# Optimization experiments

Hardware: AMD Instinct MI355X
Metric: run time of the kernel (lower is better)

The kernel has to match this reference:

```python
import jax, jax.numpy as jnp
import numpy as np

B, H, W, C = 8, 28, 28, 1024
NH = 16
HD = C // NH          # head dim 64
HID = 4 * C           # mlp hidden 4096
BC = C // 2           # bottleneck channels 512
SCALE = HD ** -0.5


def setup_inputs() -> dict:
    key = jax.random.key(0)
    ks = iter(jax.random.split(key, 32))
    def rn(shape, s=0.02):
        return jax.random.normal(next(ks), shape, jnp.float32) * s
    return dict(
        x=jax.random.normal(next(ks), (B, H, W, C), jnp.float32),
        norm1_w=jnp.ones((C,), jnp.float32), norm1_b=jnp.zeros((C,), jnp.float32),
        qkv_w=rn((C, 3 * C)), qkv_b=jnp.zeros((3 * C,), jnp.float32),
        proj_w=rn((C, C)), proj_b=jnp.zeros((C,), jnp.float32),
        rel_h=rn((2 * H - 1, HD)), rel_w=rn((2 * W - 1, HD)),
        norm2_w=jnp.ones((C,), jnp.float32), norm2_b=jnp.zeros((C,), jnp.float32),
        fc1_w=rn((C, HID)), fc1_b=jnp.zeros((HID,), jnp.float32),
        fc2_w=rn((HID, C)), fc2_b=jnp.zeros((C,), jnp.float32),
        conv1_w=rn((1, 1, C, BC)), ln1_w=jnp.ones((BC,), jnp.float32), ln1_b=jnp.zeros((BC,), jnp.float32),
        conv2_w=rn((3, 3, BC, BC)), ln2_w=jnp.ones((BC,), jnp.float32), ln2_b=jnp.zeros((BC,), jnp.float32),
        conv3_w=rn((1, 1, BC, C)), ln3_w=rn((C,)), ln3_b=rn((C,)),
    )


def _ln(x, w, b, eps):
    # layernorm over last axis (channels in NHWC)
    m = jnp.mean(x, -1, keepdims=True)
    v = jnp.mean((x - m) ** 2, -1, keepdims=True)
    return (x - m) * jax.lax.rsqrt(v + eps) * w + b


def _conv(x, w, pad):
    return jax.lax.conv_general_dilated(
        x, w, (1, 1), pad, dimension_numbers=('NHWC', 'HWIO', 'NHWC'))


def _gelu(x):
    return jax.nn.gelu(x, approximate=False)


def _block_forward(x, norm1_w, norm1_b, qkv_w, qkv_b, proj_w, proj_b,
                   rel_h, rel_w, norm2_w, norm2_b, fc1_w, fc1_b, fc2_w, fc2_b,
                   conv1_w, ln1_w, ln1_b, conv2_w, ln2_w, ln2_b, conv3_w, ln3_w, ln3_b):
    S = H * W
    shortcut = x
    xn = _ln(x, norm1_w, norm1_b, 1e-5)

    # ---- attention with decomposed relative position bias ----
    qkv = xn.reshape(B, S, C) @ qkv_w + qkv_b                 # [B,S,3C]
    qkv = qkv.reshape(B, S, 3, NH, HD).transpose(2, 0, 3, 1, 4)  # [3,B,nh,S,hd]
    q, k, v = qkv[0], qkv[1], qkv[2]
    attn = jnp.einsum('bnsd,bntd->bnst', q * SCALE, k)        # [B,nh,S,S]

    idx_h = jnp.arange(H)[:, None] - jnp.arange(H)[None, :] + (H - 1)
    idx_w = jnp.arange(W)[:, None] - jnp.arange(W)[None, :] + (W - 1)
    Rh = rel_h[idx_h]   # [H,H,hd]
    Rw = rel_w[idx_w]   # [W,W,hd]
    qr = q.reshape(B, NH, H, W, HD)
    bias_h = jnp.einsum('bnhwd,hkd->bnhwk', qr, Rh)           # [B,nh,H,W,H]
    bias_w = jnp.einsum('bnhwd,wkd->bnhwk', qr, Rw)           # [B,nh,H,W,W]
    attn = (attn.reshape(B, NH, H, W, H, W)
            + bias_h[..., :, None] + bias_w[..., None, :]).reshape(B, NH, S, S)

    attn = jax.nn.softmax(attn, axis=-1)
    out = jnp.einsum('bnst,bntd->bnsd', attn, v)              # [B,nh,S,hd]
    out = out.transpose(0, 2, 1, 3).reshape(B, H, W, C)
    out = out @ proj_w + proj_b

    x = shortcut + out

    # ---- MLP ----
    xn = _ln(x, norm2_w, norm2_b, 1e-5)
    x = x + (_gelu(xn.reshape(B, S, C) @ fc1_w + fc1_b) @ fc2_w + fc2_b).reshape(B, H, W, C)

    # ---- residual bottleneck conv (channel LayerNorm, eps=1e-6) ----
    out = _conv(x, conv1_w, 'VALID')
    out = _gelu(_ln(out, ln1_w, ln1_b, 1e-6))
    out = _conv(out, conv2_w, ((1, 1), (1, 1)))
    out = _gelu(_ln(out, ln2_w, ln2_b, 1e-6))
    out = _conv(out, conv3_w, 'VALID')
    out = _ln(out, ln3_w, ln3_b, 1e-6)
    return x + out


def reference(x, norm1_w, norm1_b, qkv_w, qkv_b, proj_w, proj_b,
              rel_h, rel_w, norm2_w, norm2_b, fc1_w, fc1_b, fc2_w, fc2_b,
              conv1_w, ln1_w, ln1_b, conv2_w, ln2_w, ln2_b, conv3_w, ln3_w, ln3_b):
    return _block_forward(x, norm1_w, norm1_b, qkv_w, qkv_b, proj_w, proj_b,
                          rel_h, rel_w, norm2_w, norm2_b, fc1_w, fc1_b, fc2_w, fc2_b,
                          conv1_w, ln1_w, ln1_b, conv2_w, ln2_w, ln2_b, conv3_w, ln3_w, ln3_b)
```

## Files before the change

kernel.cpp:

```cpp
#include <hip/hip_runtime.h>
#include <cstdint>
#include <cstddef>

using u16 = unsigned short;
using u32 = unsigned int;

__device__ __forceinline__ float bf2f(u16 u){
  union { u32 i; float f; } x; x.i = ((u32)u) << 16; return x.f;
}
__device__ __forceinline__ u16 f2bf(float f){
  union { float f; u32 i; } x; x.f = f;
  u32 r = x.i + 0x7fffu + ((x.i >> 16) & 1u);
  return (u16)(r >> 16);
}
__device__ __forceinline__ float gelu_f(float x){
  return 0.5f * x * (1.0f + erff(x * 0.70710678118654752f));
}
__device__ __forceinline__ void gld16(const void* g, void* l){
  __builtin_amdgcn_global_load_lds((__attribute__((address_space(1))) void*)(void*)g,
                                   (__attribute__((address_space(3))) void*)l, 16, 0, 0);
}

typedef __bf16 bf16x8 __attribute__((ext_vector_type(8)));
typedef float  f32x4  __attribute__((ext_vector_type(4)));

__global__ __launch_bounds__(256) void k_transpose(const float* __restrict__ src,
                                                   u16* __restrict__ dst, int R, int C){
  __shared__ u16 tile[32][33];
  int bx = blockIdx.x * 32;
  int by = blockIdx.y * 32;
  int tx = threadIdx.x & 31;
  int ty = threadIdx.x >> 5;
  for (int r = ty; r < 32; r += 8)
    tile[r][tx] = f2bf(src[(size_t)(by + r) * C + bx + tx]);
  __syncthreads();
  for (int r = ty; r < 32; r += 8)
    dst[(size_t)(bx + r) * R + by + tx] = tile[tx][r];
}

template<bool IN_F32, bool DO_GELU>
__global__ __launch_bounds__(256) void k_layernorm(const void* __restrict__ inp,
    const float* __restrict__ w, const float* __restrict__ bsh,
    u16* __restrict__ out, int cols, float eps){
  int row = blockIdx.x, t = threadIdx.x;
  size_t base = (size_t)row * cols;
  const float* inf = (const float*)inp;
  const u16*  inb = (const u16*)inp;
  float v[4];
  int ep = cols >> 8;
  float s = 0.f, ss = 0.f;
  for (int e = 0; e < ep; ++e){
    int idx = t + (e << 8);
    float x = IN_F32 ? inf[base + idx] : bf2f(inb[base + idx]);
    v[e] = x; s += x; ss += x * x;
  }
#pragma unroll
  for (int off = 1; off < 64; off <<= 1){
    s  += __shfl_xor(s, off, 64);
    ss += __shfl_xor(ss, off, 64);
  }
  __shared__ float red[8];
  int wv = t >> 6;
  if ((t & 63) == 0){ red[wv] = s; red[4 + wv] = ss; }
  __syncthreads();
  s  = red[0] + red[1] + red[2] + red[3];
  ss = red[4] + red[5] + red[6] + red[7];
  float inv = 1.f / (float)cols;
  float mean = s * inv;
  float var = ss * inv - mean * mean;
  float rs = rsqrtf(var + eps);
  for (int e = 0; e < ep; ++e){
    int idx = t + (e << 8);
    float y = (v[e] - mean) * rs * w[idx] + bsh[idx];
    if (DO_GELU) y = gelu_f(y);
    out[base + idx] = f2bf(y);
  }
}

__global__ __launch_bounds__(256) void k_final(const u16* __restrict__ c3,
    const u16* __restrict__ x2, const float* __restrict__ w,
    const float* __restrict__ bsh, float* __restrict__ out){
  int row = blockIdx.x, t = threadIdx.x;
  size_t base = (size_t)row << 10;
  float v[4];
  float s = 0.f, ss = 0.f;
#pragma unroll
  for (int e = 0; e < 4; ++e){
    int idx = t + (e << 8);
    float x = bf2f(c3[base + idx]);
    v[e] = x; s += x; ss += x * x;
  }
#pragma unroll
  for (int off = 1; off < 64; off <<= 1){
    s  += __shfl_xor(s, off, 64);
    ss += __shfl_xor(ss, off, 64);
  }
  __shared__ float red[8];
  int wv = t >> 6;
  if ((t & 63) == 0){ red[wv] = s; red[4 + wv] = ss; }
  __syncthreads();
  s  = red[0] + red[1] + red[2] + red[3];
  ss = red[4] + red[5] + red[6] + red[7];
  float mean = s * (1.f/1024.f);
  float var = ss * (1.f/1024.f) - mean * mean;
  float rs = rsqrtf(var + 1e-6f);
#pragma unroll
  for (int e = 0; e < 4; ++e){
    int idx = t + (e << 8);
    float y = (v[e] - mean) * rs * w[idx] + bsh[idx];
    out[base + idx] = bf2f(x2[base + idx]) + y;
  }
}

template<bool BIAS, bool GELU, bool RES, bool OUTB, bool OUTF>
__global__ __launch_bounds__(256, 2) void k_gemm(
    const u16* __restrict__ A, const u16* __restrict__ Bt,
    const float* __restrict__ bias, const float* __restrict__ resf,
    u16* __restrict__ outb, float* __restrict__ outf, int N, int K)
{
  __shared__ __align__(16) u16 As[128 * 32];
  __shared__ __align__(16) u16 Bs[128 * 32];
  int t = threadIdx.x, lane = t & 63, wv = t >> 6;
  int m0 = blockIdx.y << 7, n0 = blockIdx.x << 7;
  int wm = (wv >> 1) << 6, wn = (wv & 1) << 6;

  f32x4 acc[4][4];
  const f32x4 z4 = {0.f, 0.f, 0.f, 0.f};
#pragma unroll
  for (int i = 0; i < 4; ++i)
#pragma unroll
    for (int j = 0; j < 4; ++j) acc[i][j] = z4;

  int srow = (wv << 5) + (lane >> 2);
  int skp  = (lane & 3) << 3;
  const u16* Ag = A  + (size_t)(m0 + srow) * K + skp;
  const u16* Bg = Bt + (size_t)(n0 + srow) * K + skp;
  u16* As0 = &As[(wv << 5) * 32];
  u16* As1 = As0 + 16 * 32;
  u16* Bs0 = &Bs[(wv << 5) * 32];
  u16* Bs1 = Bs0 + 16 * 32;
  const size_t rowskip = (size_t)16 * K;

  int fr = lane & 15, fq = (lane >> 4) << 3;

  for (int k0 = 0; k0 < K; k0 += 32){
    gld16(Ag + k0, As0);
    gld16(Ag + rowskip + k0, As1);
    gld16(Bg + k0, Bs0);
    gld16(Bg + rowskip + k0, Bs1);
    __syncthreads();
    bf16x8 af[4], bfr[4];
#pragma unroll
    for (int i = 0; i < 4; ++i)
      af[i] = *(const bf16x8*)&As[(wm + i * 16 + fr) * 32 + fq];
#pragma unroll
    for (int j = 0; j < 4; ++j)
      bfr[j] = *(const bf16x8*)&Bs[(wn + j * 16 + fr) * 32 + fq];
#pragma unroll
    for (int i = 0; i < 4; ++i)
#pragma unroll
      for (int j = 0; j < 4; ++j)
        acc[i][j] = __builtin_amdgcn_mfma_f32_16x16x32_bf16(af[i], bfr[j], acc[i][j], 0, 0, 0);
    __syncthreads();
  }

  int rr = (lane >> 4) << 2;
  int cc = lane & 15;
#pragma unroll
  for (int i = 0; i < 4; ++i)
#pragma unroll
    for (int j = 0; j < 4; ++j){
      int gc = n0 + wn + j * 16 + cc;
      float bb = BIAS ? bias[gc] : 0.f;
#pragma unroll
      for (int r = 0; r < 4; ++r){
        int gr = m0 + wm + i * 16 + rr + r;
        size_t idx = (size_t)gr * N + gc;
        float vv = acc[i][j][r] + bb;
        if (RES) vv += resf[idx];
        if (GELU) vv = gelu_f(vv);
        if (OUTF) outf[idx] = vv;
        if (OUTB) outb[idx] = f2bf(vv);
      }
    }
}

#define ATT_STR 72
__global__ __launch_bounds__(256, 3) void k_attn3(const u16* __restrict__ qkv,
    const float* __restrict__ relh, const float* __restrict__ relw,
    u16* __restrict__ out)
{
  __shared__ __align__(16) u16 k_s[64 * ATT_STR];
  __shared__ __align__(16) u16 vT_s[80 * ATT_STR];
  __shared__ __align__(16) u16 p_s[128 * ATT_STR];
  __shared__ u16 gh_s[128 * 28];
  __shared__ u16 gw_s[128 * 28];

  const int t = threadIdx.x, lane = t & 63, wv = t >> 6;
  int id = blockIdx.x;
  int xr = id & 7, rest = id >> 3;
  int qt = rest % 7, gg = rest / 7;
  int bnh = xr + (gg << 3);
  const int b = bnh >> 4, nh = bnh & 15;
  const int q0 = qt << 7;
  const size_t rowbase = (size_t)b * 784;
  const int wq0 = wv << 5;
  const int fr = lane & 15;
  const int fq = lane >> 4;

  u16* rh_s = p_s;
  u16* rw_s = p_s + 64 * ATT_STR;
  {
    int row = t >> 2, c0 = (t & 3) << 4;
    u16 bh_[16], bw_[16];
    if (row < 55){
      const float* ph = relh + row * 64 + c0;
      const float* pw = relw + row * 64 + c0;
#pragma unroll
      for (int e = 0; e < 16; ++e){ bh_[e] = f2bf(ph[e]); bw_[e] = f2bf(pw[e]); }
    } else {
#pragma unroll
      for (int e = 0; e < 16; ++e){ bh_[e] = 0; bw_[e] = 0; }
    }
    *(uint4*)&rh_s[row * ATT_STR + c0]     = *(uint4*)bh_;
    *(uint4*)&rh_s[row * ATT_STR + c0 + 8] = *(uint4*)(bh_ + 8);
    *(uint4*)&rw_s[row * ATT_STR + c0]     = *(uint4*)bw_;
    *(uint4*)&rw_s[row * ATT_STR + c0 + 8] = *(uint4*)(bw_ + 8);
    for (int idx = t; idx < 16 * ATT_STR; idx += 256){
      int rr = idx / ATT_STR, cc = idx - rr * ATT_STR;
      vT_s[(64 + rr) * ATT_STR + cc] = (rr == 0 && cc < 64) ? (u16)0x3f80 : (u16)0;
    }
  }

  bf16x8 qf[2][2];
#pragma unroll
  for (int mf = 0; mf < 2; ++mf)
#pragma unroll
    for (int ks = 0; ks < 2; ++ks){
      int row = q0 + wq0 + mf * 16 + fr;
      if (row < 784){
        qf[mf][ks] = *(const bf16x8*)(qkv + (rowbase + row) * 3072 + nh * 64 + fq * 8 + ks * 32);
      } else {
        uint4 z = {0u,0u,0u,0u}; qf[mf][ks] = *(bf16x8*)&z;
      }
    }
  __syncthreads();

  const f32x4 z4 = {0.f,0.f,0.f,0.f};
#pragma unroll
  for (int which = 0; which < 2; ++which){
    const u16* rs = which ? rw_s : rh_s;
    f32x4 G[2][4];
#pragma unroll
    for (int mf = 0; mf < 2; ++mf)
#pragma unroll
      for (int nf = 0; nf < 4; ++nf) G[mf][nf] = z4;
#pragma unroll
    for (int nf = 0; nf < 4; ++nf){
      bf16x8 rf0 = *(const bf16x8*)&rs[(nf * 16 + fr) * ATT_STR + fq * 8];
      bf16x8 rf1 = *(const bf16x8*)&rs[(nf * 16 + fr) * ATT_STR + fq * 8 + 32];
#pragma unroll
      for (int mf = 0; mf < 2; ++mf){
        G[mf][nf] = __builtin_amdgcn_mfma_f32_16x16x32_bf16(qf[mf][0], rf0, G[mf][nf], 0, 0, 0);
        G[mf][nf] = __builtin_amdgcn_mfma_f32_16x16x32_bf16(qf[mf][1], rf1, G[mf][nf], 0, 0, 0);
      }
    }
    u16* gt = which ? gw_s : gh_s;
#pragma unroll
    for (int mf = 0; mf < 2; ++mf)
#pragma unroll
      for (int r = 0; r < 4; ++r){
        int lr = wq0 + mf * 16 + fq * 4 + r;
        int grow = q0 + lr;
        int hq = grow / 28;
        int coord = which ? (grow - hq * 28) : hq;
#pragma unroll
        for (int nf = 0; nf < 4; ++nf){
          int j = nf * 16 + fr;
          int kk = coord + 27 - j;
          if ((unsigned)kk < 28u) gt[lr * 28 + kk] = f2bf(G[mf][nf][r]);
        }
      }
  }
  __syncthreads();

  f32x4 acc[2][5];
#pragma unroll
  for (int mf = 0; mf < 2; ++mf)
#pragma unroll
    for (int nf = 0; nf < 5; ++nf) acc[mf][nf] = z4;

  for (int kt = 0; kt < 13; ++kt){
    __syncthreads();
    {
      int krow = lane;
      int d0 = wv << 4;
      int jg = (kt << 6) + krow;
      uint4 kv0 = {0u,0u,0u,0u}, kv1 = {0u,0u,0u,0u};
      uint4 vv0 = {0u,0u,0u,0u}, vv1 = {0u,0u,0u,0u};
      if (jg < 784){
        const u16* kp = qkv + (rowbase + jg) * 3072 + 1024 + nh * 64 + d0;
        kv0 = *(const uint4*)kp; kv1 = *(const uint4*)(kp + 8);
        vv0 = *(const uint4*)(kp + 1024); vv1 = *(const uint4*)(kp + 1032);
      }
      *(uint4*)&k_s[krow * ATT_STR + d0]     = kv0;
      *(uint4*)&k_s[krow * ATT_STR + d0 + 8] = kv1;
      u16 vbuf[16];
      *(uint4*)vbuf = vv0; *(uint4*)(vbuf + 8) = vv1;
#pragma unroll
      for (int e = 0; e < 16; ++e) vT_s[(d0 + e) * ATT_STR + krow] = vbuf[e];
    }
    __syncthreads();

    f32x4 S[2][4];
#pragma unroll
    for (int nf = 0; nf < 4; ++nf){
      bf16x8 kf0 = *(const bf16x8*)&k_s[(nf * 16 + fr) * ATT_STR + fq * 8];
      bf16x8 kf1 = *(const bf16x8*)&k_s[(nf * 16 + fr) * ATT_STR + fq * 8 + 32];
#pragma unroll
      for (int mf = 0; mf < 2; ++mf){
        f32x4 s = z4;
        s = __builtin_amdgcn_mfma_f32_16x16x32_bf16(qf[mf][0], kf0, s, 0, 0, 0);
        s = __builtin_amdgcn_mfma_f32_16x16x32_bf16(qf[mf][1], kf1, s, 0, 0, 0);
        S[mf][nf] = s;
      }
    }

    int hj[4], wj[4]; bool val[4];
#pragma unroll
    for (int nf = 0; nf < 4; ++nf){
      int jg = (kt << 6) + nf * 16 + fr;
      int h = jg / 28;
      hj[nf] = h; wj[nf] = jg - h * 28; val[nf] = (jg < 784);
    }
#pragma unroll
    for (int mf = 0; mf < 2; ++mf)
#pragma unroll
      for (int r = 0; r < 4; ++r){
        int lr = wq0 + mf * 16 + fq * 4 + r;
#pragma unroll
        for (int nf = 0; nf < 4; ++nf){
          float p = 0.f;
          if (val[nf]){
            float bias = bf2f(gh_s[lr * 28 + hj[nf]]) + bf2f(gw_s[lr * 28 + wj[nf]]);
            p = __expf(fmaf(0.125f, S[mf][nf][r], bias));
          }
          p_s[lr * ATT_STR + nf * 16 + fr] = f2bf(p);
        }
      }

#pragma unroll
    for (int ks = 0; ks < 2; ++ks){
      bf16x8 pf0 = *(const bf16x8*)&p_s[(wq0 + fr) * ATT_STR + fq * 8 + ks * 32];
      bf16x8 pf1 = *(const bf16x8*)&p_s[(wq0 + 16 + fr) * ATT_STR + fq * 8 + ks * 32];
#pragma unroll
      for (int nf = 0; nf < 5; ++nf){
        bf16x8 vf = *(const bf16x8*)&vT_s[(nf * 16 + fr) * ATT_STR + fq * 8 + ks * 32];
        acc[0][nf] = __builtin_amdgcn_mfma_f32_16x16x32_bf16(pf0, vf, acc[0][nf], 0, 0, 0);
        acc[1][nf] = __builtin_amdgcn_mfma_f32_16x16x32_bf16(pf1, vf, acc[1][nf], 0, 0, 0);
      }
    }
  }

#pragma unroll
  for (int mf = 0; mf < 2; ++mf)
#pragma unroll
    for (int r = 0; r < 4; ++r){
      float l = __shfl(acc[mf][4][r], lane & 48, 64);
      int row = q0 + wq0 + mf * 16 + fq * 4 + r;
      if (row < 784){
        float inv = 1.f / l;
        u16* dp = out + (rowbase + row) * 1024 + nh * 64 + fr;
#pragma unroll
        for (int nf = 0; nf < 4; ++nf)
          dp[nf * 16] = f2bf(acc[mf][nf][r] * inv);
      }
    }
}

__global__ __launch_bounds__(256) void k_im2col(const u16* __restrict__ g, u16* __restrict__ im){
  int idx = blockIdx.x * 256 + threadIdx.x;
  int p  = idx / 576;
  int c8 = idx - p * 576;
  int k0 = c8 << 3;
  int t9 = k0 >> 9;
  int ci = k0 & 511;
  int ky = t9 / 3, kx = t9 - ky * 3;
  int bb = p / 784;
  int s = p - bb * 784;
  int h = s / 28, w = s - h * 28;
  int hh = h + ky - 1, ww = w + kx - 1;
  uint4 val = make_uint4(0u, 0u, 0u, 0u);
  if ((unsigned)hh < 28u && (unsigned)ww < 28u)
    val = *(const uint4*)&g[(((size_t)(bb * 28 + hh)) * 28 + ww) * 512 + ci];
  *(uint4*)&im[(size_t)p * 4608 + k0] = val;
}

extern "C" void kernel_launch(void* const* d_in, const int* in_sizes, int n_in,
                              void* d_out, int out_size, void* d_ws, size_t ws_size,
                              hipStream_t stream)
{
  (void)in_sizes; (void)n_in; (void)out_size; (void)ws_size;
  const float* x      = (const float*)d_in[0];
  const float* n1w    = (const float*)d_in[1];
  const float* n1b    = (const float*)d_in[2];
  const float* qkv_w  = (const float*)d_in[3];
  const float* qkv_b  = (const float*)d_in[4];
  const float* proj_w = (const float*)d_in[5];
  const float* proj_b = (const float*)d_in[6];
  const float* rel_h  = (const float*)d_in[7];
  const float* rel_w  = (const float*)d_in[8];
  const float* n2w    = (const float*)d_in[9];
  const float* n2b    = (const float*)d_in[10];
  const float* fc1_w  = (const float*)d_in[11];
  const float* fc1_b  = (const float*)d_in[12];
  const float* fc2_w  = (const float*)d_in[13];
  const float* fc2_b  = (const float*)d_in[14];
  const float* c1w    = (const float*)d_in[15];
  const float* l1w    = (const float*)d_in[16];
  const float* l1b    = (const float*)d_in[17];
  const float* c2w    = (const float*)d_in[18];
  const float* l2w    = (const float*)d_in[19];
  const float* l2b    = (const float*)d_in[20];
  const float* c3w    = (const float*)d_in[21];
  const float* l3w    = (const float*)d_in[22];
  const float* l3b    = (const float*)d_in[23];

  char* ws = (char*)d_ws;
  size_t off = 0;
  auto alloc = [&](size_t bytes) -> void* {
    void* p = ws + off; off += (bytes + 255) & ~(size_t)255; return p;
  };
  const size_t M = 6272;
  u16* qkvT  = (u16*)alloc((size_t)3072 * 1024 * 2);
  u16* projT = (u16*)alloc((size_t)1024 * 1024 * 2);
  u16* fc1T  = (u16*)alloc((size_t)4096 * 1024 * 2);
  u16* fc2T  = (u16*)alloc((size_t)1024 * 4096 * 2);
  u16* c1T   = (u16*)alloc((size_t)512 * 1024 * 2);
  u16* c2T   = (u16*)alloc((size_t)512 * 4608 * 2);
  u16* c3T   = (u16*)alloc((size_t)1024 * 512 * 2);
  u16* qkvbuf = (u16*)alloc(M * 3072 * 2);
  u16* attn   = (u16*)alloc(M * 1024 * 2);
  u16* xn     = (u16*)alloc(M * 1024 * 2);
  float* x1   = (float*)alloc(M * 1024 * 4);
  u16* x2b    = (u16*)alloc(M * 1024 * 2);
  u16* c1buf  = (u16*)alloc(M * 512 * 2);
  u16* g1buf  = (u16*)alloc(M * 512 * 2);
  u16* hmlp   = qkvbuf;
  u16* im     = qkvbuf;
  u16* xn2    = xn;
  u16* c2buf  = c1buf;
  u16* g2buf  = g1buf;
  u16* c3buf  = attn;

  dim3 blk(256);
  k_transpose<<<dim3(3072/32, 1024/32), blk, 0, stream>>>(qkv_w, qkvT, 1024, 3072);
  k_transpose<<<dim3(1024/32, 1024/32), blk, 0, stream>>>(proj_w, projT, 1024, 1024);
  k_transpose<<<dim3(4096/32, 1024/32), blk, 0, stream>>>(fc1_w, fc1T, 1024, 4096);
  k_transpose<<<dim3(1024/32, 4096/32), blk, 0, stream>>>(fc2_w, fc2T, 4096, 1024);
  k_transpose<<<dim3(512/32, 1024/32),  blk, 0, stream>>>(c1w, c1T, 1024, 512);
  k_transpose<<<dim3(512/32, 4608/32),  blk, 0, stream>>>(c2w, c2T, 4608, 512);
  k_transpose<<<dim3(1024/32, 512/32),  blk, 0, stream>>>(c3w, c3T, 512, 1024);

  k_layernorm<true,false><<<6272, blk, 0, stream>>>(x, n1w, n1b, xn, 1024, 1e-5f);
  k_gemm<true,false,false,true,false><<<dim3(24,49), blk, 0, stream>>>(
      xn, qkvT, qkv_b, nullptr, qkvbuf, nullptr, 3072, 1024);
  k_attn3<<<896, blk, 0, stream>>>(qkvbuf, rel_h, rel_w, attn);
  k_gemm<true,false,true,false,true><<<dim3(8,49), blk, 0, stream>>>(
      attn, projT, proj_b, x, nullptr, x1, 1024, 1024);
  k_layernorm<true,false><<<6272, blk, 0, stream>>>(x1, n2w, n2b, xn2, 1024, 1e-5f);
  k_gemm<true,true,false,true,false><<<dim3(32,49), blk, 0, stream>>>(
      xn2, fc1T, fc1_b, nullptr, hmlp, nullptr, 4096, 1024);
  k_gemm<true,false,true,true,false><<<dim3(8,49), blk, 0, stream>>>(
      hmlp, fc2T, fc2_b, x1, x2b, nullptr, 1024, 4096);
  k_gemm<false,false,false,true,false><<<dim3(4,49), blk, 0, stream>>>(
      x2b, c1T, nullptr, nullptr, c1buf, nullptr, 512, 1024);
  k_layernorm<false,true><<<6272, blk, 0, stream>>>(c1buf, l1w, l1b, g1buf, 512, 1e-6f);
  k_im2col<<<14112, blk, 0, stream>>>(g1buf, im);
  k_gemm<false,false,false,true,false><<<dim3(4,49), blk, 0, stream>>>(
      im, c2T, nullptr, nullptr, c2buf, nullptr, 512, 4608);
  k_layernorm<false,true><<<6272, blk, 0, stream>>>(c2buf, l2w, l2b, g2buf, 512, 1e-6f);
  k_gemm<false,false,false,true,false><<<dim3(8,49), blk, 0, stream>>>(
      g2buf, c3T, nullptr, nullptr, c3buf, nullptr, 1024, 512);
  k_final<<<6272, blk, 0, stream>>>(c3buf, x2b, l3w, l3b, (float*)d_out);
}
```

Measured before the change: 756.9 us.

## Stream K and pre-transposed V from global in attention, dropping LDS staging

```diff
diff --git a/kernel.cpp b/kernel.cpp
--- a/kernel.cpp
+++ b/kernel.cpp
@@ -23,6 +23,7 @@
 
 typedef __bf16 bf16x8 __attribute__((ext_vector_type(8)));
 typedef float  f32x4  __attribute__((ext_vector_type(4)));
+typedef u16    u16x4  __attribute__((ext_vector_type(4)));
 
 __global__ __launch_bounds__(256) void k_transpose(const float* __restrict__ src,
                                                    u16* __restrict__ dst, int R, int C){
@@ -185,16 +186,43 @@
     }
 }
 
+__global__ __launch_bounds__(256) void k_vtrans(const u16* __restrict__ qkv, u16* __restrict__ vtg){
+  __shared__ u32 tile[64][33];
+  int bnh = blockIdx.x;
+  int st  = blockIdx.y;
+  int b = bnh >> 4, nh = bnh & 15;
+  int t = threadIdx.x;
+  int tx = t & 31;
+  int ty = t >> 5;
+  const u16* src = qkv + (size_t)b * 784 * 3072 + 2048 + nh * 64;
+  int s0 = st << 6;
+  for (int r = ty; r < 64; r += 8){
+    int s = s0 + r;
+    u32 val = 0u;
+    if (s < 784) val = *(const u32*)(src + (size_t)s * 3072 + tx * 2);
+    tile[r][tx] = val;
+  }
+  __syncthreads();
+  u16* dst = vtg + (size_t)bnh * 64 * 832 + s0;
+  for (int d = ty; d < 64; d += 8){
+    u32 lo = tile[2 * tx][d >> 1];
+    u32 hi = tile[2 * tx + 1][d >> 1];
+    u16 a  = (d & 1) ? (u16)(lo >> 16) : (u16)lo;
+    u16 bb = (d & 1) ? (u16)(hi >> 16) : (u16)hi;
+    u32 pk = (u32)a | ((u32)bb << 16);
+    *(u32*)(dst + (size_t)d * 832 + 2 * tx) = pk;
+  }
+}
+
 #define ATT_STR 72
-__global__ __launch_bounds__(256, 3) void k_attn3(const u16* __restrict__ qkv,
+#define GSTR 132
+__global__ __launch_bounds__(256, 4) void k_attn4(const u16* __restrict__ qkv,
     const float* __restrict__ relh, const float* __restrict__ relw,
-    u16* __restrict__ out)
+    const u16* __restrict__ vtg, u16* __restrict__ out)
 {
-  __shared__ __align__(16) u16 k_s[64 * ATT_STR];
-  __shared__ __align__(16) u16 vT_s[80 * ATT_STR];
   __shared__ __align__(16) u16 p_s[128 * ATT_STR];
-  __shared__ u16 gh_s[128 * 28];
-  __shared__ u16 gw_s[128 * 28];
+  __shared__ __align__(16) u16 gh_t[28 * GSTR];
+  __shared__ __align__(16) u16 gw_t[28 * GSTR];
 
   const int t = threadIdx.x, lane = t & 63, wv = t >> 6;
   int id = blockIdx.x;
@@ -226,10 +254,6 @@
     *(uint4*)&rh_s[row * ATT_STR + c0 + 8] = *(uint4*)(bh_ + 8);
     *(uint4*)&rw_s[row * ATT_STR + c0]     = *(uint4*)bw_;
     *(uint4*)&rw_s[row * ATT_STR + c0 + 8] = *(uint4*)(bw_ + 8);
-    for (int idx = t; idx < 16 * ATT_STR; idx += 256){
-      int rr = idx / ATT_STR, cc = idx - rr * ATT_STR;
-      vT_s[(64 + rr) * ATT_STR + cc] = (rr == 0 && cc < 64) ? (u16)0x3f80 : (u16)0;
-    }
   }
 
   bf16x8 qf[2][2];
@@ -265,7 +289,7 @@
         G[mf][nf] = __builtin_amdgcn_mfma_f32_16x16x32_bf16(qf[mf][1], rf1, G[mf][nf], 0, 0, 0);
       }
     }
-    u16* gt = which ? gw_s : gh_s;
+    u16* gt = which ? gw_t : gh_t;
 #pragma unroll
     for (int mf = 0; mf < 2; ++mf)
 #pragma unroll
@@ -278,7 +302,7 @@
         for (int nf = 0; nf < 4; ++nf){
           int j = nf * 16 + fr;
           int kk = coord + 27 - j;
-          if ((unsigned)kk < 28u) gt[lr * 28 + kk] = f2bf(G[mf][nf][r]);
+          if ((unsigned)kk < 28u) gt[kk * GSTR + lr] = f2bf(G[mf][nf][r]);
         }
       }
   }
@@ -290,33 +314,24 @@
 #pragma unroll
     for (int nf = 0; nf < 5; ++nf) acc[mf][nf] = z4;
 
+  u16 onesu[8];
+#pragma unroll
+  for (int e = 0; e < 8; ++e) onesu[e] = 0x3f80;
+  bf16x8 onesf = *(bf16x8*)onesu;
+
+  const u16* kgb = qkv + rowbase * 3072 + 1024 + nh * 64 + fq * 8;
+  const u16* vgb = vtg + ((size_t)bnh * 64 + fr) * 832 + fq * 8;
+
   for (int kt = 0; kt < 13; ++kt){
-    __syncthreads();
-    {
-      int krow = lane;
-      int d0 = wv << 4;
-      int jg = (kt << 6) + krow;
-      uint4 kv0 = {0u,0u,0u,0u}, kv1 = {0u,0u,0u,0u};
-      uint4 vv0 = {0u,0u,0u,0u}, vv1 = {0u,0u,0u,0u};
-      if (jg < 784){
-        const u16* kp = qkv + (rowbase + jg) * 3072 + 1024 + nh * 64 + d0;
-        kv0 = *(const uint4*)kp; kv1 = *(const uint4*)(kp + 8);
-        vv0 = *(const uint4*)(kp + 1024); vv1 = *(const uint4*)(kp + 1032);
-      }
-      *(uint4*)&k_s[krow * ATT_STR + d0]     = kv0;
-      *(uint4*)&k_s[krow * ATT_STR + d0 + 8] = kv1;
-      u16 vbuf[16];
-      *(uint4*)vbuf = vv0; *(uint4*)(vbuf + 8) = vv1;
-#pragma unroll
-      for (int e = 0; e < 16; ++e) vT_s[(d0 + e) * ATT_STR + krow] = vbuf[e];
-    }
-    __syncthreads();
-
+    const int ktb = kt << 6;
     f32x4 S[2][4];
 #pragma unroll
     for (int nf = 0; nf < 4; ++nf){
-      bf16x8 kf0 = *(const bf16x8*)&k_s[(nf * 16 + fr) * ATT_STR + fq * 8];
-      bf16x8 kf1 = *(const bf16x8*)&k_s[(nf * 16 + fr) * ATT_STR + fq * 8 + 32];
+      int jg = ktb + nf * 16 + fr;
+      int jc = jg < 784 ? jg : 783;
+      const u16* kp = kgb + (size_t)jc * 3072;
+      bf16x8 kf0 = *(const bf16x8*)kp;
+      bf16x8 kf1 = *(const bf16x8*)(kp + 32);
 #pragma unroll
       for (int mf = 0; mf < 2; ++mf){
         f32x4 s = z4;
@@ -329,36 +344,40 @@
     int hj[4], wj[4]; bool val[4];
 #pragma unroll
     for (int nf = 0; nf < 4; ++nf){
-      int jg = (kt << 6) + nf * 16 + fr;
+      int jg = ktb + nf * 16 + fr;
       int h = jg / 28;
       hj[nf] = h; wj[nf] = jg - h * 28; val[nf] = (jg < 784);
     }
-#pragma unroll
-    for (int mf = 0; mf < 2; ++mf)
-#pragma unroll
-      for (int r = 0; r < 4; ++r){
-        int lr = wq0 + mf * 16 + fq * 4 + r;
-#pragma unroll
-        for (int nf = 0; nf < 4; ++nf){
+
+#pragma unroll
+    for (int mf = 0; mf < 2; ++mf){
+      int lrb = wq0 + mf * 16 + fq * 4;
+#pragma unroll
+      for (int nf = 0; nf < 4; ++nf){
+        u16x4 h4 = *(const u16x4*)&gh_t[hj[nf] * GSTR + lrb];
+        u16x4 w4 = *(const u16x4*)&gw_t[wj[nf] * GSTR + lrb];
+#pragma unroll
+        for (int r = 0; r < 4; ++r){
           float p = 0.f;
-          if (val[nf]){
-            float bias = bf2f(gh_s[lr * 28 + hj[nf]]) + bf2f(gw_s[lr * 28 + wj[nf]]);
-            p = __expf(fmaf(0.125f, S[mf][nf][r], bias));
-          }
-          p_s[lr * ATT_STR + nf * 16 + fr] = f2bf(p);
+          if (val[nf])
+            p = __expf(fmaf(0.125f, S[mf][nf][r], bf2f(h4[r]) + bf2f(w4[r])));
+          p_s[(lrb + r) * ATT_STR + nf * 16 + fr] = f2bf(p);
         }
       }
+    }
 
 #pragma unroll
     for (int ks = 0; ks < 2; ++ks){
       bf16x8 pf0 = *(const bf16x8*)&p_s[(wq0 + fr) * ATT_STR + fq * 8 + ks * 32];
       bf16x8 pf1 = *(const bf16x8*)&p_s[(wq0 + 16 + fr) * ATT_STR + fq * 8 + ks * 32];
 #pragma unroll
-      for (int nf = 0; nf < 5; ++nf){
-        bf16x8 vf = *(const bf16x8*)&vT_s[(nf * 16 + fr) * ATT_STR + fq * 8 + ks * 32];
+      for (int nf = 0; nf < 4; ++nf){
+        bf16x8 vf = *(const bf16x8*)(vgb + (size_t)(nf * 16) * 832 + ktb + ks * 32);
         acc[0][nf] = __builtin_amdgcn_mfma_f32_16x16x32_bf16(pf0, vf, acc[0][nf], 0, 0, 0);
         acc[1][nf] = __builtin_amdgcn_mfma_f32_16x16x32_bf16(pf1, vf, acc[1][nf], 0, 0, 0);
       }
+      acc[0][4] = __builtin_amdgcn_mfma_f32_16x16x32_bf16(pf0, onesf, acc[0][4], 0, 0, 0);
+      acc[1][4] = __builtin_amdgcn_mfma_f32_16x16x32_bf16(pf1, onesf, acc[1][4], 0, 0, 0);
     }
   }
 
@@ -366,10 +385,9 @@
   for (int mf = 0; mf < 2; ++mf)
 #pragma unroll
     for (int r = 0; r < 4; ++r){
-      float l = __shfl(acc[mf][4][r], lane & 48, 64);
       int row = q0 + wq0 + mf * 16 + fq * 4 + r;
       if (row < 784){
-        float inv = 1.f / l;
+        float inv = 1.f / acc[mf][4][r];
         u16* dp = out + (rowbase + row) * 1024 + nh * 64 + fr;
 #pragma unroll
         for (int nf = 0; nf < 4; ++nf)
@@ -452,6 +470,7 @@
   u16* c2buf  = c1buf;
   u16* g2buf  = g1buf;
   u16* c3buf  = attn;
+  u16* vtg    = (u16*)x1;
 
   dim3 blk(256);
   k_transpose<<<dim3(3072/32, 1024/32), blk, 0, stream>>>(qkv_w, qkvT, 1024, 3072);
@@ -465,7 +484,8 @@
   k_layernorm<true,false><<<6272, blk, 0, stream>>>(x, n1w, n1b, xn, 1024, 1e-5f);
   k_gemm<true,false,false,true,false><<<dim3(24,49), blk, 0, stream>>>(
       xn, qkvT, qkv_b, nullptr, qkvbuf, nullptr, 3072, 1024);
-  k_attn3<<<896, blk, 0, stream>>>(qkvbuf, rel_h, rel_w, attn);
+  k_vtrans<<<dim3(128, 13), blk, 0, stream>>>(qkvbuf, vtg);
+  k_attn4<<<896, blk, 0, stream>>>(qkvbuf, rel_h, rel_w, vtg, attn);
   k_gemm<true,false,true,false,true><<<dim3(8,49), blk, 0, stream>>>(
       attn, projT, proj_b, x, nullptr, x1, 1024, 1024);
   k_layernorm<true,false><<<6272, blk, 0, stream>>>(x1, n2w, n2b, xn2, 1024, 1e-5f);
```

Result: no change. 757.4 us (+0.1%).
